# Kernel optimization log

Hardware: AMD Instinct MI355X
Metric: run time of the kernel (lower is better)

## Reference

```python
import jax, jax.numpy as jnp
import numpy as np

D_MODEL = 1024
NUM_HEADS = 16
DEPTH = D_MODEL // NUM_HEADS


def setup_inputs() -> dict:
    key = jax.random.key(0)
    ks = jax.random.split(key, 10)
    B, LQ, LK = 4, 2048, 2048
    # xavier_uniform bound for square [d,d] weight
    bound = float(np.sqrt(6.0 / (D_MODEL + D_MODEL)))
    def w(k):
        return jax.random.uniform(k, (D_MODEL, D_MODEL), jnp.float32, -bound, bound)
    return {
        "query": jax.random.normal(ks[0], (B, LQ, D_MODEL), jnp.float32),
        "value": jax.random.normal(ks[1], (B, LK, D_MODEL), jnp.float32),
        "wq": w(ks[2]), "bq": jnp.zeros((D_MODEL,), jnp.float32),
        "wk": w(ks[3]), "bk": jnp.zeros((D_MODEL,), jnp.float32),
        "wv": w(ks[4]), "bv": jnp.zeros((D_MODEL,), jnp.float32),
        "wo": w(ks[5]), "bo": jnp.zeros((D_MODEL,), jnp.float32),
    }


def _split_heads(x, B):
    # [B, L, d_model] -> [B, H, L, depth]
    return x.reshape(B, -1, NUM_HEADS, DEPTH).transpose(0, 2, 1, 3)


def reference(query, value, wq, bq, wk, bk, wv, bv, wo, bo):
    B = query.shape[0]
    # torch nn.Linear: y = x @ W.T + b
    q = _split_heads(query @ wq.T + bq, B)          # [B,H,Lq,depth]
    k = _split_heads(value @ wk.T + bk, B)          # [B,H,Lk,depth]
    v = _split_heads(value @ wv.T + bv, B)          # [B,H,Lk,depth]
    scale = jnp.sqrt(jnp.asarray(DEPTH, dtype=q.dtype))
    scores = jnp.einsum("bhqd,bhkd->bhqk", q, k) / scale
    attn = jax.nn.softmax(scores, axis=-1)
    ctx = jnp.einsum("bhqk,bhkd->bhqd", attn, v)    # [B,H,Lq,depth]
    ctx = ctx.transpose(0, 2, 1, 3).reshape(B, -1, D_MODEL)
    return ctx @ wo.T + bo
```

## Files before the change

kernel.cpp:

```cpp
#include <hip/hip_runtime.h>
#include <hip/hip_bf16.h>

typedef unsigned short u16;
typedef unsigned int u32;
typedef __attribute__((ext_vector_type(8))) short bf16x8;
typedef __attribute__((ext_vector_type(4))) float f32x4;

#define MFMA16(a, b, c) __builtin_amdgcn_mfma_f32_16x16x32_bf16(a, b, c, 0, 0, 0)

#define QSCALE 0.18033688011112042f

__device__ inline u16 f2b(float f) {
    union { float f; unsigned int i; } v;
    v.f = f;
    unsigned int r = v.i + 0x7fffu + ((v.i >> 16) & 1u);
    return (u16)(r >> 16);
}
__device__ inline u32 fbits(float f) {
    union { float f; u32 i; } v; v.f = f; return v.i;
}
__device__ inline u32 pack2_trunc(float f0, float f1) {
    return __builtin_amdgcn_perm(fbits(f1), fbits(f0), 0x07060302u);
}

__device__ inline void glds16(const u16* g, u16* l) {
    __builtin_amdgcn_global_load_lds(
        (const __attribute__((address_space(1))) unsigned int*)g,
        (__attribute__((address_space(3))) unsigned int*)l, 16, 0, 0);
}

__global__ __launch_bounds__(256) void cvt_f32_bf16(
    const float* __restrict__ x, u16* __restrict__ y, int n)
{
    int i = (blockIdx.x * 256 + threadIdx.x) * 8;
    if (i >= n) return;
    float4 a = *(const float4*)(x + i);
    float4 b = *(const float4*)(x + i + 4);
    u16 o[8] = { f2b(a.x), f2b(a.y), f2b(a.z), f2b(a.w),
                 f2b(b.x), f2b(b.y), f2b(b.z), f2b(b.w) };
    *(uint4*)(y + i) = *(uint4*)o;
}

__global__ __launch_bounds__(256) void gemm_proj(
    const u16* __restrict__ qb, const u16* __restrict__ vb,
    const u16* __restrict__ wqb, const u16* __restrict__ wkb,
    const u16* __restrict__ wvb,
    const float* __restrict__ bq, const float* __restrict__ bk,
    const float* __restrict__ bv,
    u16* __restrict__ Qp, u16* __restrict__ Kp, u16* __restrict__ Vp,
    int M, int K)
{
    const int sel = blockIdx.y >> 3;
    const int n0 = (blockIdx.y & 7) * 128;
    const u16* A = sel ? vb : qb;
    const u16* W = sel == 0 ? wqb : (sel == 1 ? wkb : wvb);
    const float* bias = sel == 0 ? bq : (sel == 1 ? bk : bv);
    u16* C = sel == 0 ? Qp : (sel == 1 ? Kp : Vp);
    const float cscale = sel == 0 ? QSCALE : 1.0f;

    __shared__ __align__(16) u16 As[128 * 32];
    __shared__ __align__(16) u16 Bs[128 * 32];

    const int tid  = threadIdx.x;
    const int wave = tid >> 6, lane = tid & 63;
    const int quad = lane >> 4, l16 = lane & 15;
    const int m0 = blockIdx.x * 128;
    const int wm = (wave >> 1) * 64, wn = (wave & 1) * 64;
    const int r0 = lane >> 2;
    const int c0 = (lane & 3) * 8;

    f32x4 acc[4][4] = {};

    for (int k0 = 0; k0 < K; k0 += 32) {
        __syncthreads();
        {
            int ra = wave * 16 + r0;
            glds16(&A[(size_t)(m0 + ra) * K + k0 + c0],      &As[ra * 32 + c0]);
            glds16(&A[(size_t)(m0 + 64 + ra) * K + k0 + c0], &As[(64 + ra) * 32 + c0]);
            glds16(&W[(size_t)(n0 + ra) * K + k0 + c0],      &Bs[ra * 32 + c0]);
            glds16(&W[(size_t)(n0 + 64 + ra) * K + k0 + c0], &Bs[(64 + ra) * 32 + c0]);
        }
        __syncthreads();

        bf16x8 af[4], bfr[4];
#pragma unroll
        for (int mi = 0; mi < 4; ++mi)
            af[mi] = *(const bf16x8*)(&As[(wm + mi * 16 + l16) * 32 + quad * 8]);
#pragma unroll
        for (int ni = 0; ni < 4; ++ni)
            bfr[ni] = *(const bf16x8*)(&Bs[(wn + ni * 16 + l16) * 32 + quad * 8]);
#pragma unroll
        for (int mi = 0; mi < 4; ++mi)
#pragma unroll
            for (int ni = 0; ni < 4; ++ni)
                acc[mi][ni] = MFMA16(af[mi], bfr[ni], acc[mi][ni]);
    }

#pragma unroll
    for (int mi = 0; mi < 4; ++mi) {
#pragma unroll
        for (int ni = 0; ni < 4; ++ni) {
            int col = n0 + wn + ni * 16 + l16;
            float bv2 = bias[col];
#pragma unroll
            for (int r = 0; r < 4; ++r) {
                int row = m0 + wm + mi * 16 + quad * 4 + r;
                C[(size_t)row * 1024 + col] = f2b((acc[mi][ni][r] + bv2) * cscale);
            }
        }
    }
}

__global__ __launch_bounds__(256) void gemm_out(
    const u16* __restrict__ A, const u16* __restrict__ B,
    const float* __restrict__ bias, float* __restrict__ C,
    int M, int N, int K)
{
    __shared__ __align__(16) u16 As[128 * 32];
    __shared__ __align__(16) u16 Bs[128 * 32];

    const int tid  = threadIdx.x;
    const int wave = tid >> 6, lane = tid & 63;
    const int quad = lane >> 4, l16 = lane & 15;
    const int m0 = blockIdx.x * 128, n0 = blockIdx.y * 128;
    const int wm = (wave >> 1) * 64, wn = (wave & 1) * 64;
    const int r0 = lane >> 2;
    const int c0 = (lane & 3) * 8;

    f32x4 acc[4][4] = {};

    for (int k0 = 0; k0 < K; k0 += 32) {
        __syncthreads();
        {
            int ra = wave * 16 + r0;
            glds16(&A[(size_t)(m0 + ra) * K + k0 + c0],      &As[ra * 32 + c0]);
            glds16(&A[(size_t)(m0 + 64 + ra) * K + k0 + c0], &As[(64 + ra) * 32 + c0]);
            glds16(&B[(size_t)(n0 + ra) * K + k0 + c0],      &Bs[ra * 32 + c0]);
            glds16(&B[(size_t)(n0 + 64 + ra) * K + k0 + c0], &Bs[(64 + ra) * 32 + c0]);
        }
        __syncthreads();

        bf16x8 af[4], bfr[4];
#pragma unroll
        for (int mi = 0; mi < 4; ++mi)
            af[mi] = *(const bf16x8*)(&As[(wm + mi * 16 + l16) * 32 + quad * 8]);
#pragma unroll
        for (int ni = 0; ni < 4; ++ni)
            bfr[ni] = *(const bf16x8*)(&Bs[(wn + ni * 16 + l16) * 32 + quad * 8]);
#pragma unroll
        for (int mi = 0; mi < 4; ++mi)
#pragma unroll
            for (int ni = 0; ni < 4; ++ni)
                acc[mi][ni] = MFMA16(af[mi], bfr[ni], acc[mi][ni]);
    }

#pragma unroll
    for (int mi = 0; mi < 4; ++mi) {
#pragma unroll
        for (int ni = 0; ni < 4; ++ni) {
            int col = n0 + wn + ni * 16 + l16;
            float bv = bias[col];
#pragma unroll
            for (int r = 0; r < 4; ++r) {
                int row = m0 + wm + mi * 16 + quad * 4 + r;
                C[(size_t)row * N + col] = acc[mi][ni][r] + bv;
            }
        }
    }
}

__global__ __launch_bounds__(256) void transpose_v(
    const u16* __restrict__ Vp, u16* __restrict__ VT)
{
    __shared__ u16 T[64 * 66];
    const int tid = threadIdx.x;
    const int l0 = blockIdx.x * 64, d0 = blockIdx.y * 64, b = blockIdx.z;

#pragma unroll
    for (int i = 0; i < 2; ++i) {
        int ch = tid + i * 256;
        int lrow = ch >> 3, c8 = (ch & 7) * 8;
        uint4 vv = *(const uint4*)(&Vp[((size_t)b * 2048 + l0 + lrow) * 1024 + d0 + c8]);
        const u16* vp = (const u16*)&vv;
#pragma unroll
        for (int j = 0; j < 8; ++j) T[lrow * 66 + c8 + j] = vp[j];
    }
    __syncthreads();
#pragma unroll
    for (int i = 0; i < 2; ++i) {
        int ch = tid + i * 256;
        int drow = ch >> 3, l8 = (ch & 7) * 8;
        u16 o[8];
#pragma unroll
        for (int j = 0; j < 8; ++j) o[j] = T[(l8 + j) * 66 + drow];
        *(uint4*)(&VT[((size_t)b * 1024 + d0 + drow) * 2048 + l0 + l8]) = *(uint4*)o;
    }
}

__global__ __launch_bounds__(256) void attn(
    const u16* __restrict__ Q, const u16* __restrict__ K,
    const u16* __restrict__ VT, u16* __restrict__ O,
    int LQ, int LK)
{
    const int tid  = threadIdx.x;
    const int wave = tid >> 6, lane = tid & 63;
    const int quad = lane >> 4, l16 = lane & 15;
    const int q0 = blockIdx.x * 256;
    const int bh = blockIdx.y;
    const int b = bh >> 4, h = bh & 15;
    const size_t qbase = ((size_t)b * LQ + q0) * 1024 + h * 64;
    const size_t kbase = ((size_t)b * LK) * 1024 + h * 64;
    const size_t vtbase = ((size_t)b * 1024 + h * 64) * 2048;

    __shared__ __align__(16) u16 Ks[64 * 72];
    __shared__ __align__(16) u16 VTs[80 * 72];
    __shared__ __align__(16) u16 Ps[4][64 * 72];

    for (int i = tid; i < 16 * 72; i += 256) VTs[64 * 72 + i] = 0x3F80;

    bf16x8 qf[4][2];
#pragma unroll
    for (int mi = 0; mi < 4; ++mi)
#pragma unroll
        for (int ks = 0; ks < 2; ++ks)
            qf[mi][ks] = *(const bf16x8*)(
                &Q[qbase + (size_t)(wave * 64 + mi * 16 + l16) * 1024 + ks * 32 + quad * 8]);

    f32x4 oacc[4][5] = {};

    for (int kt = 0; kt < LK; kt += 64) {
        __syncthreads();
#pragma unroll
        for (int i = 0; i < 2; ++i) {
            int ch = tid + i * 256;
            int row = ch >> 3, c8 = (ch & 7) * 8;
            *(uint4*)(&Ks[row * 72 + c8]) =
                *(const uint4*)(&K[kbase + (size_t)(kt + row) * 1024 + c8]);
            *(uint4*)(&VTs[row * 72 + c8]) =
                *(const uint4*)(&VT[vtbase + (size_t)row * 2048 + kt + c8]);
        }
        __syncthreads();

        f32x4 st[4][4] = {};
#pragma unroll
        for (int ks = 0; ks < 2; ++ks) {
            bf16x8 kf[4];
#pragma unroll
            for (int ni = 0; ni < 4; ++ni)
                kf[ni] = *(const bf16x8*)(&Ks[(ni * 16 + l16) * 72 + ks * 32 + quad * 8]);
#pragma unroll
            for (int ni = 0; ni < 4; ++ni)
#pragma unroll
                for (int mi = 0; mi < 4; ++mi)
                    st[ni][mi] = MFMA16(kf[ni], qf[mi][ks], st[ni][mi]);
        }

#pragma unroll
        for (int mi = 0; mi < 4; ++mi)
#pragma unroll
            for (int ni = 0; ni < 4; ++ni) {
                float p0 = __builtin_amdgcn_exp2f(st[ni][mi][0]);
                float p1 = __builtin_amdgcn_exp2f(st[ni][mi][1]);
                float p2 = __builtin_amdgcn_exp2f(st[ni][mi][2]);
                float p3 = __builtin_amdgcn_exp2f(st[ni][mi][3]);
                uint2 w;
                w.x = pack2_trunc(p0, p1);
                w.y = pack2_trunc(p2, p3);
                *(uint2*)(&Ps[wave][(mi * 16 + l16) * 72 + ni * 16 + quad * 4]) = w;
            }

#pragma unroll
        for (int ks = 0; ks < 2; ++ks) {
            bf16x8 vf[5];
#pragma unroll
            for (int nd = 0; nd < 5; ++nd)
                vf[nd] = *(const bf16x8*)(&VTs[(nd * 16 + l16) * 72 + ks * 32 + quad * 8]);
#pragma unroll
            for (int mi = 0; mi < 4; ++mi) {
                bf16x8 pf = *(const bf16x8*)(&Ps[wave][(mi * 16 + l16) * 72 + ks * 32 + quad * 8]);
#pragma unroll
                for (int nd = 0; nd < 5; ++nd)
                    oacc[mi][nd] = MFMA16(pf, vf[nd], oacc[mi][nd]);
            }
        }
    }

#pragma unroll
    for (int mi = 0; mi < 4; ++mi)
#pragma unroll
        for (int r = 0; r < 4; ++r) {
            float inv = 1.0f / oacc[mi][4][r];
            int row = q0 + wave * 64 + mi * 16 + quad * 4 + r;
            size_t rb = ((size_t)b * LQ + row) * 1024 + h * 64;
#pragma unroll
            for (int nd = 0; nd < 4; ++nd)
                O[rb + nd * 16 + l16] = f2b(oacc[mi][nd][r] * inv);
        }
}

extern "C" void kernel_launch(void* const* d_in, const int* in_sizes, int n_in,
                              void* d_out, int out_size, void* d_ws, size_t ws_size,
                              hipStream_t stream) {
    const float* query = (const float*)d_in[0];
    const float* value = (const float*)d_in[1];
    const float* wq = (const float*)d_in[2];
    const float* bq = (const float*)d_in[3];
    const float* wk = (const float*)d_in[4];
    const float* bk = (const float*)d_in[5];
    const float* wv = (const float*)d_in[6];
    const float* bv = (const float*)d_in[7];
    const float* wo = (const float*)d_in[8];
    const float* bo = (const float*)d_in[9];

    const int B = 4, LQ = 2048, LK = 2048, D = 1024;
    const int M = B * LQ;
    const int mat = M * D;
    const int wsz = D * D;

    u16* ws  = (u16*)d_ws;
    u16* qb  = ws;
    u16* vb  = qb + mat;
    u16* wqb = vb + mat;
    u16* wkb = wqb + wsz;
    u16* wvb = wkb + wsz;
    u16* wob = wvb + wsz;
    u16* Qp  = wob + wsz;
    u16* Kp  = Qp + mat;
    u16* Vp  = Kp + mat;
    u16* VT  = Vp + mat;
    u16* Cp  = Vp;

    dim3 blk(256);

    cvt_f32_bf16<<<dim3(mat / 2048), blk, 0, stream>>>(query, qb, mat);
    cvt_f32_bf16<<<dim3(mat / 2048), blk, 0, stream>>>(value, vb, mat);
    cvt_f32_bf16<<<dim3(wsz / 2048), blk, 0, stream>>>(wq, wqb, wsz);
    cvt_f32_bf16<<<dim3(wsz / 2048), blk, 0, stream>>>(wk, wkb, wsz);
    cvt_f32_bf16<<<dim3(wsz / 2048), blk, 0, stream>>>(wv, wvb, wsz);
    cvt_f32_bf16<<<dim3(wsz / 2048), blk, 0, stream>>>(wo, wob, wsz);

    gemm_proj<<<dim3(M / 128, 24), blk, 0, stream>>>(
        qb, vb, wqb, wkb, wvb, bq, bk, bv, Qp, Kp, Vp, M, D);

    transpose_v<<<dim3(32, 16, 4), blk, 0, stream>>>(Vp, VT);

    attn<<<dim3(LQ / 256, B * 16), blk, 0, stream>>>(Qp, Kp, VT, Cp, LQ, LK);

    gemm_out<<<dim3(M / 128, D / 128), blk, 0, stream>>>(Cp, wob, bo, (float*)d_out, M, D, D);
}
```

Measured before the change: 349.5 us.

## Widen GEMM k-step to 64 and halve attention P buffer for occupancy

Both GEMM kernels now load two 32-wide k slices per barrier pair, so each iteration covers 64 of K and there are half as many __syncthreads. Shared memory per GEMM block doubles in exchange. The attention kernel writes and consumes the probability tile in two 32-column halves, which halves the per-wave P buffer in LDS. It also adds a launch_bounds min-blocks hint of 4 to raise occupancy, at the risk of register pressure or spills. Reusing the same P buffer for both halves without an explicit wave barrier depends on in-order execution within the wave.

```diff
diff --git a/kernel.cpp b/kernel.cpp
--- a/kernel.cpp
+++ b/kernel.cpp
@@ -40,6 +40,42 @@
                  f2b(b.x), f2b(b.y), f2b(b.z), f2b(b.w) };
     *(uint4*)(y + i) = *(uint4*)o;
 }
+
+#define GEMM_KLOOP(Aptr, Bptr)                                                  \
+    for (int k0 = 0; k0 < K; k0 += 64) {                                        \
+        __syncthreads();                                                        \
+        {                                                                       \
+            int ra = wave * 16 + r0;                                            \
+            _Pragma("unroll")                                                   \
+            for (int s = 0; s < 2; ++s) {                                       \
+                int ks0 = k0 + s * 32;                                          \
+                glds16(&Aptr[(size_t)(m0 + ra) * K + ks0 + c0],                 \
+                       &As[s][ra * 32 + c0]);                                   \
+                glds16(&Aptr[(size_t)(m0 + 64 + ra) * K + ks0 + c0],            \
+                       &As[s][(64 + ra) * 32 + c0]);                            \
+                glds16(&Bptr[(size_t)(n0 + ra) * K + ks0 + c0],                 \
+                       &Bs[s][ra * 32 + c0]);                                   \
+                glds16(&Bptr[(size_t)(n0 + 64 + ra) * K + ks0 + c0],            \
+                       &Bs[s][(64 + ra) * 32 + c0]);                            \
+            }                                                                   \
+        }                                                                       \
+        __syncthreads();                                                        \
+        _Pragma("unroll")                                                       \
+        for (int s = 0; s < 2; ++s) {                                           \
+            bf16x8 af[4], bfr[4];                                               \
+            _Pragma("unroll")                                                   \
+            for (int mi = 0; mi < 4; ++mi)                                      \
+                af[mi] = *(const bf16x8*)(&As[s][(wm + mi * 16 + l16) * 32 + quad * 8]); \
+            _Pragma("unroll")                                                   \
+            for (int ni = 0; ni < 4; ++ni)                                      \
+                bfr[ni] = *(const bf16x8*)(&Bs[s][(wn + ni * 16 + l16) * 32 + quad * 8]); \
+            _Pragma("unroll")                                                   \
+            for (int mi = 0; mi < 4; ++mi)                                      \
+                _Pragma("unroll")                                               \
+                for (int ni = 0; ni < 4; ++ni)                                  \
+                    acc[mi][ni] = MFMA16(af[mi], bfr[ni], acc[mi][ni]);         \
+        }                                                                       \
+    }
 
 __global__ __launch_bounds__(256) void gemm_proj(
     const u16* __restrict__ qb, const u16* __restrict__ vb,
@@ -58,8 +94,8 @@
     u16* C = sel == 0 ? Qp : (sel == 1 ? Kp : Vp);
     const float cscale = sel == 0 ? QSCALE : 1.0f;
 
-    __shared__ __align__(16) u16 As[128 * 32];
-    __shared__ __align__(16) u16 Bs[128 * 32];
+    __shared__ __align__(16) u16 As[2][128 * 32];
+    __shared__ __align__(16) u16 Bs[2][128 * 32];
 
     const int tid  = threadIdx.x;
     const int wave = tid >> 6, lane = tid & 63;
@@ -71,30 +107,7 @@
 
     f32x4 acc[4][4] = {};
 
-    for (int k0 = 0; k0 < K; k0 += 32) {
-        __syncthreads();
-        {
-            int ra = wave * 16 + r0;
-            glds16(&A[(size_t)(m0 + ra) * K + k0 + c0],      &As[ra * 32 + c0]);
-            glds16(&A[(size_t)(m0 + 64 + ra) * K + k0 + c0], &As[(64 + ra) * 32 + c0]);
-            glds16(&W[(size_t)(n0 + ra) * K + k0 + c0],      &Bs[ra * 32 + c0]);
-            glds16(&W[(size_t)(n0 + 64 + ra) * K + k0 + c0], &Bs[(64 + ra) * 32 + c0]);
-        }
-        __syncthreads();
-
-        bf16x8 af[4], bfr[4];
-#pragma unroll
-        for (int mi = 0; mi < 4; ++mi)
-            af[mi] = *(const bf16x8*)(&As[(wm + mi * 16 + l16) * 32 + quad * 8]);
-#pragma unroll
-        for (int ni = 0; ni < 4; ++ni)
-            bfr[ni] = *(const bf16x8*)(&Bs[(wn + ni * 16 + l16) * 32 + quad * 8]);
-#pragma unroll
-        for (int mi = 0; mi < 4; ++mi)
-#pragma unroll
-            for (int ni = 0; ni < 4; ++ni)
-                acc[mi][ni] = MFMA16(af[mi], bfr[ni], acc[mi][ni]);
-    }
+    GEMM_KLOOP(A, W)
 
 #pragma unroll
     for (int mi = 0; mi < 4; ++mi) {
@@ -116,8 +129,8 @@
     const float* __restrict__ bias, float* __restrict__ C,
     int M, int N, int K)
 {
-    __shared__ __align__(16) u16 As[128 * 32];
-    __shared__ __align__(16) u16 Bs[128 * 32];
+    __shared__ __align__(16) u16 As[2][128 * 32];
+    __shared__ __align__(16) u16 Bs[2][128 * 32];
 
     const int tid  = threadIdx.x;
     const int wave = tid >> 6, lane = tid & 63;
@@ -129,30 +142,7 @@
 
     f32x4 acc[4][4] = {};
 
-    for (int k0 = 0; k0 < K; k0 += 32) {
-        __syncthreads();
-        {
-            int ra = wave * 16 + r0;
-            glds16(&A[(size_t)(m0 + ra) * K + k0 + c0],      &As[ra * 32 + c0]);
-            glds16(&A[(size_t)(m0 + 64 + ra) * K + k0 + c0], &As[(64 + ra) * 32 + c0]);
-            glds16(&B[(size_t)(n0 + ra) * K + k0 + c0],      &Bs[ra * 32 + c0]);
-            glds16(&B[(size_t)(n0 + 64 + ra) * K + k0 + c0], &Bs[(64 + ra) * 32 + c0]);
-        }
-        __syncthreads();
-
-        bf16x8 af[4], bfr[4];
-#pragma unroll
-        for (int mi = 0; mi < 4; ++mi)
-            af[mi] = *(const bf16x8*)(&As[(wm + mi * 16 + l16) * 32 + quad * 8]);
-#pragma unroll
-        for (int ni = 0; ni < 4; ++ni)
-            bfr[ni] = *(const bf16x8*)(&Bs[(wn + ni * 16 + l16) * 32 + quad * 8]);
-#pragma unroll
-        for (int mi = 0; mi < 4; ++mi)
-#pragma unroll
-            for (int ni = 0; ni < 4; ++ni)
-                acc[mi][ni] = MFMA16(af[mi], bfr[ni], acc[mi][ni]);
-    }
+    GEMM_KLOOP(A, B)
 
 #pragma unroll
     for (int mi = 0; mi < 4; ++mi) {
@@ -197,7 +187,7 @@
     }
 }
 
-__global__ __launch_bounds__(256) void attn(
+__global__ __launch_bounds__(256, 4) void attn(
     const u16* __restrict__ Q, const u16* __restrict__ K,
     const u16* __restrict__ VT, u16* __restrict__ O,
     int LQ, int LK)
@@ -214,7 +204,7 @@
 
     __shared__ __align__(16) u16 Ks[64 * 72];
     __shared__ __align__(16) u16 VTs[80 * 72];
-    __shared__ __align__(16) u16 Ps[4][64 * 72];
+    __shared__ __align__(16) u16 Ps[4][64 * 36];
 
     for (int i = tid; i < 16 * 72; i += 256) VTs[64 * 72 + i] = 0x3F80;
 
@@ -256,28 +246,28 @@
         }
 
 #pragma unroll
-        for (int mi = 0; mi < 4; ++mi)
-#pragma unroll
-            for (int ni = 0; ni < 4; ++ni) {
-                float p0 = __builtin_amdgcn_exp2f(st[ni][mi][0]);
-                float p1 = __builtin_amdgcn_exp2f(st[ni][mi][1]);
-                float p2 = __builtin_amdgcn_exp2f(st[ni][mi][2]);
-                float p3 = __builtin_amdgcn_exp2f(st[ni][mi][3]);
-                uint2 w;
-                w.x = pack2_trunc(p0, p1);
-                w.y = pack2_trunc(p2, p3);
-                *(uint2*)(&Ps[wave][(mi * 16 + l16) * 72 + ni * 16 + quad * 4]) = w;
-            }
-
-#pragma unroll
-        for (int ks = 0; ks < 2; ++ks) {
+        for (int kh = 0; kh < 2; ++kh) {
+#pragma unroll
+            for (int mi = 0; mi < 4; ++mi)
+#pragma unroll
+                for (int nj = 0; nj < 2; ++nj) {
+                    int ni = kh * 2 + nj;
+                    float p0 = __builtin_amdgcn_exp2f(st[ni][mi][0]);
+                    float p1 = __builtin_amdgcn_exp2f(st[ni][mi][1]);
+                    float p2 = __builtin_amdgcn_exp2f(st[ni][mi][2]);
+                    float p3 = __builtin_amdgcn_exp2f(st[ni][mi][3]);
+                    uint2 w;
+                    w.x = pack2_trunc(p0, p1);
+                    w.y = pack2_trunc(p2, p3);
+                    *(uint2*)(&Ps[wave][(mi * 16 + l16) * 36 + nj * 16 + quad * 4]) = w;
+                }
             bf16x8 vf[5];
 #pragma unroll
             for (int nd = 0; nd < 5; ++nd)
-                vf[nd] = *(const bf16x8*)(&VTs[(nd * 16 + l16) * 72 + ks * 32 + quad * 8]);
+                vf[nd] = *(const bf16x8*)(&VTs[(nd * 16 + l16) * 72 + kh * 32 + quad * 8]);
 #pragma unroll
             for (int mi = 0; mi < 4; ++mi) {
-                bf16x8 pf = *(const bf16x8*)(&Ps[wave][(mi * 16 + l16) * 72 + ks * 32 + quad * 8]);
+                bf16x8 pf = *(const bf16x8*)(&Ps[wave][(mi * 16 + l16) * 36 + quad * 8]);
 #pragma unroll
                 for (int nd = 0; nd < 5; ++nd)
                     oacc[mi][nd] = MFMA16(pf, vf[nd], oacc[mi][nd]);
```

Result: slower. 775.6 us (+122.0%).
